# Kernel tuning notes

Measured on AMD Instinct MI355X. Metric: run time of the kernel, lower is better.

Reference implementation:

```python
import jax, jax.numpy as jnp
import numpy as np

EMB_DIM = 2048
USER_DIM = 16 + 112  # 128
NUM_EXPERTS = 64
TOP_K = 8
N_TOKENS = 131072


def setup_inputs() -> dict:
    key = jax.random.key(0)
    k1, k2, k3, k4 = jax.random.split(key, 4)
    h = jax.random.normal(k1, (N_TOKENS, EMB_DIM), dtype=jnp.float32)
    u = jax.random.normal(k2, (N_TOKENS, USER_DIM), dtype=jnp.float32)
    fan_in = EMB_DIM + USER_DIM
    bound = 1.0 / np.sqrt(fan_in)
    # nn.Linear params: weight [E, emb+user], bias [E]
    W = jax.random.uniform(k3, (NUM_EXPERTS, fan_in), minval=-bound, maxval=bound, dtype=jnp.float32)
    b = jax.random.uniform(k4, (NUM_EXPERTS,), minval=-bound, maxval=bound, dtype=jnp.float32)
    return {"h": h, "u": u, "W": W, "b": b}


def reference(h, u, W, b):
    # router logits: concat along feature dim then linear -> [N, E]
    x = jnp.concatenate([h, u], axis=-1)
    g = jnp.einsum("nf,ef->ne", x, W) + b
    w = jax.nn.softmax(g, axis=-1)
    E = w.shape[-1]
    k = TOP_K
    if k is not None and k > 0 and k < E:
        _, idx = jax.lax.top_k(w, k)                      # [N, k] int32
        mask = jax.nn.one_hot(idx, E, dtype=w.dtype).sum(-2)  # [N, E] 0/1
        w = w * mask
        w = w / (w.sum(axis=-1, keepdims=True) + 1e-9)
    return w
```

## Files before the change

kernel.cpp:

```cpp
#include <hip/hip_runtime.h>
#include <math.h>

#define NTOK 131072
#define EMB  2048
#define UDIM 128
#define KDIM 2176
#define NE   64
#define TOPK 8

#define BM     128
#define BK     64
#define NCHUNK 34
#define NKSTEP 68
#define LSTR   65
#define MARGIN 1e-4f
#define WPLANE ((size_t)NKSTEP * 64 * 32)

typedef short bf16x8 __attribute__((ext_vector_type(8)));
typedef float f32x4  __attribute__((ext_vector_type(4)));

union FragU { uint4 u; bf16x8 v; };

__device__ __forceinline__ unsigned rnbf(unsigned u) {
    return u + 0x7FFFu + ((u >> 16) & 1u);
}

__device__ __forceinline__ void cvt8(const float4 a, const float4 b,
                                     uint4& hi, uint4& lo) {
    const float x[8] = {a.x, a.y, a.z, a.w, b.x, b.y, b.z, b.w};
    unsigned hh[4], ll[4];
    #pragma unroll
    for (int p = 0; p < 4; ++p) {
        const unsigned u0 = __float_as_uint(x[2*p]);
        const unsigned u1 = __float_as_uint(x[2*p+1]);
        const unsigned r0 = rnbf(u0), r1 = rnbf(u1);
        hh[p] = (r0 >> 16) | (r1 & 0xFFFF0000u);
        const float h0 = __uint_as_float(r0 & 0xFFFF0000u);
        const float h1 = __uint_as_float(r1 & 0xFFFF0000u);
        const unsigned s0 = rnbf(__float_as_uint(x[2*p]   - h0));
        const unsigned s1 = rnbf(__float_as_uint(x[2*p+1] - h1));
        ll[p] = (s0 >> 16) | (s1 & 0xFFFF0000u);
    }
    hi = make_uint4(hh[0], hh[1], hh[2], hh[3]);
    lo = make_uint4(ll[0], ll[1], ll[2], ll[3]);
}

__device__ __forceinline__ void gll16(const void* gsrc, void* ldst) {
    __builtin_amdgcn_global_load_lds(
        (const __attribute__((address_space(1))) void*)gsrc,
        (__attribute__((address_space(3))) void*)ldst, 16, 0, 0);
}

__global__ __launch_bounds__(256)
void prep_w(const float* __restrict__ W,
            unsigned short* __restrict__ wh,
            unsigned short* __restrict__ wl)
{
    const int t = blockIdx.x * 256 + threadIdx.x;
    if (t >= NKSTEP * 64 * 4) return;
    const int lk = t & 3, e = (t >> 2) & 63, ks = t >> 8;
    const float* p = W + (size_t)e * KDIM + ks * 32 + lk * 8;
    const float4 a = *reinterpret_cast<const float4*>(p);
    const float4 c = *reinterpret_cast<const float4*>(p + 4);
    uint4 hi, lo;
    cvt8(a, c, hi, lo);
    const size_t di = (size_t)ks * 2048 +
                      ((size_t)((e >> 4) * 64 + (e & 15) + 16 * lk)) * 8;
    *reinterpret_cast<uint4*>(wh + di) = hi;
    *reinterpret_cast<uint4*>(wl + di) = lo;
}

__global__ void zero_flags(int* flagbuf) {
    if (threadIdx.x == 0 && blockIdx.x == 0) flagbuf[0] = 0;
}

__global__ __launch_bounds__(256, 4)
void gate_main(const float* __restrict__ h,
               const float* __restrict__ u,
               const unsigned short* __restrict__ wh,
               const unsigned short* __restrict__ wl,
               const float* __restrict__ b,
               int* __restrict__ flagbuf,
               float* __restrict__ out)
{
    __shared__ __align__(16) char smem[33536];
    __shared__ int flaglist[BM];
    __shared__ int nflag;

    const int tid  = threadIdx.x;
    const int lane = tid & 63;
    const int wid  = tid >> 6;
    const int bm   = blockIdx.x * BM;
    const int lrow = lane & 15;
    const int lk   = lane >> 4;

    if (tid == 0) nflag = 0;

    f32x4 acc[2][4];
    #pragma unroll
    for (int mi = 0; mi < 2; ++mi)
        #pragma unroll
        for (int ni = 0; ni < 4; ++ni)
            acc[mi][ni] = (f32x4){0.f, 0.f, 0.f, 0.f};

    float4 xr[8];

    auto loadX = [&](int c) {
        const bool  fh  = (c < 32);
        const float* src = fh ? h : u;
        const int   ld  = fh ? EMB : UDIM;
        const int   kb  = c * BK - (fh ? 0 : EMB);
        #pragma unroll
        for (int mi = 0; mi < 2; ++mi) {
            const size_t ro = (size_t)(bm + wid*32 + mi*16 + lrow) * ld + kb + lk*8;
            #pragma unroll
            for (int s = 0; s < 2; ++s) {
                xr[mi*4 + s*2 + 0] = *reinterpret_cast<const float4*>(src + ro + s*32);
                xr[mi*4 + s*2 + 1] = *reinterpret_cast<const float4*>(src + ro + s*32 + 4);
            }
        }
    };

    auto stageW = [&](int c, int pb) {
        const char* hsrc = (const char*)wh + (size_t)c * 8192;
        const char* lsrc = (const char*)wl + (size_t)c * 8192;
        char* dst = smem + pb * 16384;
        #pragma unroll
        for (int i = 0; i < 2; ++i) {
            const int o = wid * 2048 + i * 1024;
            gll16(hsrc + o + lane * 16, dst + o);
            gll16(lsrc + o + lane * 16, dst + 8192 + o);
        }
    };

    auto computeChunk = [&](int c, int pb) {
        const uint4* wb = reinterpret_cast<const uint4*>(smem + pb * 16384);
        #pragma unroll
        for (int s = 0; s < 2; ++s) {
            FragU bh[4], bl[4];
            #pragma unroll
            for (int ni = 0; ni < 4; ++ni) {
                bh[ni].u = wb[s*256 + ni*64 + lane];
                bl[ni].u = wb[512 + s*256 + ni*64 + lane];
            }
            FragU ah[2], al[2];
            cvt8(xr[0*4 + s*2], xr[0*4 + s*2 + 1], ah[0].u, al[0].u);
            cvt8(xr[1*4 + s*2], xr[1*4 + s*2 + 1], ah[1].u, al[1].u);
            if (s == 1 && c + 1 < NCHUNK) loadX(c + 1);
            #pragma unroll
            for (int mi = 0; mi < 2; ++mi)
                #pragma unroll
                for (int ni = 0; ni < 4; ++ni) {
                    acc[mi][ni] = __builtin_amdgcn_mfma_f32_16x16x32_bf16(ah[mi].v, bh[ni].v, acc[mi][ni], 0, 0, 0);
                    acc[mi][ni] = __builtin_amdgcn_mfma_f32_16x16x32_bf16(ah[mi].v, bl[ni].v, acc[mi][ni], 0, 0, 0);
                    acc[mi][ni] = __builtin_amdgcn_mfma_f32_16x16x32_bf16(al[mi].v, bh[ni].v, acc[mi][ni], 0, 0, 0);
                }
        }
    };

    stageW(0, 0);
    loadX(0);
    __syncthreads();

    #pragma unroll 1
    for (int c = 0; c < NCHUNK; ++c) {
        if (c + 1 < NCHUNK) stageW(c + 1, (c + 1) & 1);
        computeChunk(c, c & 1);
        __syncthreads();
    }

    float* ls = reinterpret_cast<float*>(smem);
    #pragma unroll
    for (int mi = 0; mi < 2; ++mi)
        #pragma unroll
        for (int ni = 0; ni < 4; ++ni) {
            const float be = b[ni*16 + lrow];
            #pragma unroll
            for (int r = 0; r < 4; ++r) {
                const int tl = wid*32 + mi*16 + lk*4 + r;
                const int e  = ni*16 + lrow;
                ls[tl * LSTR + e] = acc[mi][ni][r] + be;
            }
        }
    __syncthreads();

    if (tid < BM) {
        float* row = ls + tid * LSTR;
        unsigned long long selm = 0ULL;
        float mx = 0.f, l8 = 0.f, l9 = 0.f;
        for (int s = 0; s < TOPK + 1; ++s) {
            float best = -1e30f; int bi = 0;
            #pragma unroll
            for (int e = 0; e < NE; ++e) {
                const float v = row[e];
                if (!((selm >> e) & 1ULL) && v > best) { best = v; bi = e; }
            }
            if (s == 0) mx = best;
            if (s < TOPK) selm |= 1ULL << bi;
            if (s == TOPK - 1) l8 = best;
            if (s == TOPK)     l9 = best;
        }
        if (l8 - l9 < MARGIN) {
            const int slot = atomicAdd(&nflag, 1);
            flaglist[slot] = tid;
        }
        float tot = 0.f, s8 = 0.f;
        #pragma unroll
        for (int e = 0; e < NE; ++e) {
            const float p = __expf(row[e] - mx);
            tot += p;
            if ((selm >> e) & 1ULL) s8 += p;
            row[e] = p;
        }
        const float inv = 1.f / (s8 + 1e-9f * tot);
        #pragma unroll
        for (int e = 0; e < NE; ++e)
            row[e] = ((selm >> e) & 1ULL) ? row[e] * inv : 0.f;
    }
    __syncthreads();

    {
        const int tx = tid & 15, ty = tid >> 4;
        #pragma unroll
        for (int r = 0; r < 8; ++r) {
            const int m = ty + r * 16;
            float4 v;
            v.x = ls[m * LSTR + tx*4 + 0];
            v.y = ls[m * LSTR + tx*4 + 1];
            v.z = ls[m * LSTR + tx*4 + 2];
            v.w = ls[m * LSTR + tx*4 + 3];
            *reinterpret_cast<float4*>(out + (size_t)(bm + m) * NE + tx*4) = v;
        }
    }

    if (tid < nflag) {
        const int slot = atomicAdd(flagbuf, 1);
        flagbuf[1 + slot] = bm + flaglist[tid];
    }
}

__global__ __launch_bounds__(256)
void gate_refine(const float* __restrict__ h,
                 const float* __restrict__ u,
                 const float* __restrict__ W,
                 const float* __restrict__ b,
                 const int* __restrict__ flagbuf,
                 float* __restrict__ out)
{
    __shared__ double dscr[576];
    const int nf = flagbuf[0];
    for (int f = blockIdx.x; f < nf; f += gridDim.x) {
        const int tok  = flagbuf[1 + f];
        const int tid  = threadIdx.x;
        const int e    = tid & 63;
        const int part = tid >> 6;
        const int ka = part * 544, kb2 = ka + 544;
        double s = 0.0;
        #pragma unroll 4
        for (int k = ka; k < kb2; ++k) {
            const float xv = (k < EMB) ? h[(size_t)tok * EMB + k]
                                       : u[(size_t)tok * UDIM + (k - EMB)];
            s = fma((double)xv, (double)W[(size_t)e * KDIM + k], s);
        }
        dscr[part * 64 + e] = s;
        __syncthreads();
        if (tid < NE) {
            const double l = dscr[tid] + dscr[64 + tid] + dscr[128 + tid] +
                             dscr[192 + tid] + (double)b[tid];
            dscr[512 + tid] = l;
        }
        __syncthreads();
        if (tid == 0) {
            double* dl = dscr + 512;
            double mx = dl[0];
            #pragma unroll
            for (int e2 = 1; e2 < NE; ++e2) mx = fmax(mx, dl[e2]);
            double tot = 0.0;
            #pragma unroll
            for (int e2 = 0; e2 < NE; ++e2) {
                const double p = exp(dl[e2] - mx);
                dl[e2] = p;
                tot += p;
            }
            double s8 = 0.0;
            for (int ss = 0; ss < TOPK; ++ss) {
                double best = -1.0; int bi = 0;
                for (int e2 = 0; e2 < NE; ++e2) {
                    const double p = dl[e2];
                    if (p > best) { best = p; bi = e2; }
                }
                s8 += best;
                dl[bi] = -best;
            }
            const double inv = 1.0 / (s8 + 1e-9 * tot);
            for (int e2 = 0; e2 < NE; ++e2) {
                const double p = dl[e2];
                out[(size_t)tok * NE + e2] = (float)((p < 0.0) ? (-p) * inv : 0.0);
            }
        }
        __syncthreads();
    }
}

extern "C" void kernel_launch(void* const* d_in, const int* in_sizes, int n_in,
                              void* d_out, int out_size, void* d_ws, size_t ws_size,
                              hipStream_t stream) {
    const float* h = (const float*)d_in[0];
    const float* u = (const float*)d_in[1];
    const float* W = (const float*)d_in[2];
    const float* b = (const float*)d_in[3];
    float* out = (float*)d_out;
    (void)in_sizes; (void)n_in; (void)out_size; (void)ws_size;

    unsigned short* wh = (unsigned short*)d_ws;
    unsigned short* wl = wh + WPLANE;
    int* flagbuf = (int*)(wl + WPLANE);

    hipLaunchKernelGGL(zero_flags, dim3(1), dim3(64), 0, stream, flagbuf);
    hipLaunchKernelGGL(prep_w, dim3(NKSTEP), dim3(256), 0, stream, W, wh, wl);
    hipLaunchKernelGGL(gate_main, dim3(NTOK / BM), dim3(256), 0, stream,
                       h, u, wh, wl, b, flagbuf, out);
    hipLaunchKernelGGL(gate_refine, dim3(256), dim3(256), 0, stream,
                       h, u, W, b, flagbuf, out);
}
```

Before: 393.7 us.

## Triple-buffer weight staging and double-depth X prefetch with explicit vmcnt barriers

Replaces the double-buffered weight staging with a three-slot ring that keeps two chunks of the split-bf16 weights in flight, and doubles the register-resident activation prefetch to 128 columns in two halves. Each half is refilled right after use. The __syncthreads calls become s_barrier guarded by partial vmcnt waits and sched_barriers, so outstanding global loads can overlap MFMA work across iterations. The cost is more LDS (48KB) and more registers, and launch bounds drop to 3 blocks per SIMD, which lowers occupancy. The hand-counted vmcnt values must match the issued load count exactly, or the pipeline reads stale data.

```diff
diff --git a/kernel.cpp b/kernel.cpp
--- a/kernel.cpp
+++ b/kernel.cpp
@@ -9,8 +9,8 @@
 #define TOPK 8
 
 #define BM     128
-#define BK     64
-#define NCHUNK 34
+#define NSUB   34
+#define NCHK   17
 #define NKSTEP 68
 #define LSTR   65
 #define MARGIN 1e-4f
@@ -74,7 +74,7 @@
     if (threadIdx.x == 0 && blockIdx.x == 0) flagbuf[0] = 0;
 }
 
-__global__ __launch_bounds__(256, 4)
+__global__ __launch_bounds__(256, 3)
 void gate_main(const float* __restrict__ h,
                const float* __restrict__ u,
                const unsigned short* __restrict__ wh,
@@ -83,7 +83,7 @@
                int* __restrict__ flagbuf,
                float* __restrict__ out)
 {
-    __shared__ __align__(16) char smem[33536];
+    __shared__ __align__(16) char smem[49152];
     __shared__ int flaglist[BM];
     __shared__ int nflag;
 
@@ -103,28 +103,12 @@
         for (int ni = 0; ni < 4; ++ni)
             acc[mi][ni] = (f32x4){0.f, 0.f, 0.f, 0.f};
 
-    float4 xr[8];
-
-    auto loadX = [&](int c) {
-        const bool  fh  = (c < 32);
-        const float* src = fh ? h : u;
-        const int   ld  = fh ? EMB : UDIM;
-        const int   kb  = c * BK - (fh ? 0 : EMB);
-        #pragma unroll
-        for (int mi = 0; mi < 2; ++mi) {
-            const size_t ro = (size_t)(bm + wid*32 + mi*16 + lrow) * ld + kb + lk*8;
-            #pragma unroll
-            for (int s = 0; s < 2; ++s) {
-                xr[mi*4 + s*2 + 0] = *reinterpret_cast<const float4*>(src + ro + s*32);
-                xr[mi*4 + s*2 + 1] = *reinterpret_cast<const float4*>(src + ro + s*32 + 4);
-            }
-        }
-    };
-
-    auto stageW = [&](int c, int pb) {
-        const char* hsrc = (const char*)wh + (size_t)c * 8192;
-        const char* lsrc = (const char*)wl + (size_t)c * 8192;
-        char* dst = smem + pb * 16384;
+    float4 xr[16];
+
+    auto stageW = [&](int g, int rb) {
+        const char* hsrc = (const char*)wh + (size_t)g * 8192;
+        const char* lsrc = (const char*)wl + (size_t)g * 8192;
+        char* dst = smem + rb * 16384;
         #pragma unroll
         for (int i = 0; i < 2; ++i) {
             const int o = wid * 2048 + i * 1024;
@@ -133,41 +117,83 @@
         }
     };
 
-    auto computeChunk = [&](int c, int pb) {
-        const uint4* wb = reinterpret_cast<const uint4*>(smem + pb * 16384);
-        #pragma unroll
-        for (int s = 0; s < 2; ++s) {
-            FragU bh[4], bl[4];
-            #pragma unroll
-            for (int ni = 0; ni < 4; ++ni) {
-                bh[ni].u = wb[s*256 + ni*64 + lane];
-                bl[ni].u = wb[512 + s*256 + ni*64 + lane];
-            }
-            FragU ah[2], al[2];
-            cvt8(xr[0*4 + s*2], xr[0*4 + s*2 + 1], ah[0].u, al[0].u);
-            cvt8(xr[1*4 + s*2], xr[1*4 + s*2 + 1], ah[1].u, al[1].u);
-            if (s == 1 && c + 1 < NCHUNK) loadX(c + 1);
-            #pragma unroll
-            for (int mi = 0; mi < 2; ++mi)
-                #pragma unroll
-                for (int ni = 0; ni < 4; ++ni) {
-                    acc[mi][ni] = __builtin_amdgcn_mfma_f32_16x16x32_bf16(ah[mi].v, bh[ni].v, acc[mi][ni], 0, 0, 0);
-                    acc[mi][ni] = __builtin_amdgcn_mfma_f32_16x16x32_bf16(ah[mi].v, bl[ni].v, acc[mi][ni], 0, 0, 0);
-                    acc[mi][ni] = __builtin_amdgcn_mfma_f32_16x16x32_bf16(al[mi].v, bh[ni].v, acc[mi][ni], 0, 0, 0);
-                }
-        }
-    };
+#define LOADX_HALF(C, H) do {                                                   \
+    const int c_ = (C);                                                         \
+    const bool fh_ = (c_ < 16);                                                 \
+    const float* src_ = fh_ ? h : u;                                            \
+    const int ld_ = fh_ ? EMB : UDIM;                                           \
+    const int kb_ = c_ * 128 - (fh_ ? 0 : EMB) + (H) * 64;                      \
+    _Pragma("unroll")                                                           \
+    for (int mi = 0; mi < 2; ++mi) {                                            \
+        const size_t ro_ = (size_t)(bm + wid*32 + mi*16 + lrow) * ld_ + kb_ + lk*8; \
+        xr[mi*8 + (H)*4 + 0] = *reinterpret_cast<const float4*>(src_ + ro_);      \
+        xr[mi*8 + (H)*4 + 1] = *reinterpret_cast<const float4*>(src_ + ro_ + 4);  \
+        xr[mi*8 + (H)*4 + 2] = *reinterpret_cast<const float4*>(src_ + ro_ + 32); \
+        xr[mi*8 + (H)*4 + 3] = *reinterpret_cast<const float4*>(src_ + ro_ + 36); \
+    }                                                                           \
+} while (0)
+
+#define COMPUTE_SUB(P, T, REFILL) do {                                          \
+    const uint4* wb_ = reinterpret_cast<const uint4*>(                          \
+        smem + ((2*(T) + (P)) % 3) * 16384);                                    \
+    _Pragma("unroll")                                                           \
+    for (int sl = 0; sl < 2; ++sl) {                                            \
+        FragU bh_[4], bl_[4];                                                   \
+        _Pragma("unroll")                                                       \
+        for (int ni = 0; ni < 4; ++ni) {                                        \
+            bh_[ni].u = wb_[sl*256 + ni*64 + lane];                             \
+            bl_[ni].u = wb_[512 + sl*256 + ni*64 + lane];                       \
+        }                                                                       \
+        FragU ah0_, al0_, ah1_, al1_;                                           \
+        cvt8(xr[((P)*2+sl)*2 + 0], xr[((P)*2+sl)*2 + 1], ah0_.u, al0_.u);       \
+        cvt8(xr[8 + ((P)*2+sl)*2 + 0], xr[8 + ((P)*2+sl)*2 + 1], ah1_.u, al1_.u); \
+        if (sl == 1 && (REFILL)) { LOADX_HALF((T) + 1, P); }                    \
+        _Pragma("unroll")                                                       \
+        for (int ni = 0; ni < 4; ++ni) {                                        \
+            acc[0][ni] = __builtin_amdgcn_mfma_f32_16x16x32_bf16(ah0_.v, bh_[ni].v, acc[0][ni], 0,0,0); \
+            acc[0][ni] = __builtin_amdgcn_mfma_f32_16x16x32_bf16(ah0_.v, bl_[ni].v, acc[0][ni], 0,0,0); \
+            acc[0][ni] = __builtin_amdgcn_mfma_f32_16x16x32_bf16(al0_.v, bh_[ni].v, acc[0][ni], 0,0,0); \
+            acc[1][ni] = __builtin_amdgcn_mfma_f32_16x16x32_bf16(ah1_.v, bh_[ni].v, acc[1][ni], 0,0,0); \
+            acc[1][ni] = __builtin_amdgcn_mfma_f32_16x16x32_bf16(ah1_.v, bl_[ni].v, acc[1][ni], 0,0,0); \
+            acc[1][ni] = __builtin_amdgcn_mfma_f32_16x16x32_bf16(al1_.v, bh_[ni].v, acc[1][ni], 0,0,0); \
+        }                                                                       \
+    }                                                                           \
+} while (0)
+
+#define SB0 __builtin_amdgcn_sched_barrier(0)
+#define BAR20 do { SB0; asm volatile("s_waitcnt vmcnt(20)" ::: "memory"); \
+                   __builtin_amdgcn_s_barrier(); SB0; } while (0)
 
     stageW(0, 0);
-    loadX(0);
+    stageW(1, 1);
+    SB0;
+    LOADX_HALF(0, 0);
+    LOADX_HALF(0, 1);
+    BAR20;
+
+    #pragma unroll 1
+    for (int t = 0; t < 16; ++t) {
+        stageW(2*t + 2, (2*t + 2) % 3);
+        SB0;
+        COMPUTE_SUB(0, t, 1);
+        BAR20;
+        stageW(2*t + 3, (2*t + 3) % 3);
+        SB0;
+        COMPUTE_SUB(1, t, 1);
+        BAR20;
+    }
+    COMPUTE_SUB(0, 16, 0);
+    SB0;
+    asm volatile("s_waitcnt vmcnt(8)" ::: "memory");
+    __builtin_amdgcn_s_barrier();
+    SB0;
+    COMPUTE_SUB(1, 16, 0);
     __syncthreads();
 
-    #pragma unroll 1
-    for (int c = 0; c < NCHUNK; ++c) {
-        if (c + 1 < NCHUNK) stageW(c + 1, (c + 1) & 1);
-        computeChunk(c, c & 1);
-        __syncthreads();
-    }
+#undef COMPUTE_SUB
+#undef LOADX_HALF
+#undef BAR20
+#undef SB0
 
     float* ls = reinterpret_cast<float*>(smem);
     #pragma unroll
```

New measurement: 471.4 us. 19.7% more time.
